# Kernel optimization log

Hardware: AMD Instinct MI355X
Metric: run time of the kernel (lower is better)

Reference implementation:

```python
import jax, jax.numpy as jnp
import numpy as np

B, T, N, F = 32, 256, 68, 64
NUM_LAYERS = 3
EPS = 1e-5


def _build_adjacency(n):
    a = np.zeros((n, n), dtype=np.float32)
    i = np.arange(n)
    a[i[1:], i[1:] - 1] = 1.0
    a[i[:-1], i[:-1] + 1] = 1.0
    return jnp.asarray(a)


def setup_inputs() -> dict:
    key = jax.random.key(0)
    ks = jax.random.split(key, 10)
    x = jax.random.normal(ks[0], (B, T, N, 2), dtype=jnp.float32)
    adj = _build_adjacency(N)  # (N, N) tridiagonal buffer (not trainable)
    W_enc = jax.random.normal(ks[1], (2, F), dtype=jnp.float32) * 0.5
    b_enc = jax.random.normal(ks[2], (F,), dtype=jnp.float32) * 0.05
    W_gnn = jax.random.normal(ks[3], (NUM_LAYERS, F, F), dtype=jnp.float32) * (1.0 / np.sqrt(F))
    b_gnn = jax.random.normal(ks[4], (NUM_LAYERS, F), dtype=jnp.float32) * 0.05
    gamma = jnp.ones((NUM_LAYERS, F), dtype=jnp.float32)
    beta = jnp.zeros((NUM_LAYERS, F), dtype=jnp.float32)
    W1 = jax.random.normal(ks[5], (F, 32), dtype=jnp.float32) * (1.0 / np.sqrt(F))
    b1 = jax.random.normal(ks[6], (32,), dtype=jnp.float32) * 0.05
    W2 = jax.random.normal(ks[7], (32, 1), dtype=jnp.float32) * (1.0 / np.sqrt(32))
    b2 = jax.random.normal(ks[8], (1,), dtype=jnp.float32) * 0.05
    return {"landmarks_sequence": x, "adj": adj, "W_enc": W_enc, "b_enc": b_enc,
            "W_gnn": W_gnn, "b_gnn": b_gnn, "gamma": gamma, "beta": beta,
            "W1": W1, "b1": b1, "W2": W2, "b2": b2}


def _layernorm(z, g, b):
    mu = jnp.mean(z, axis=-1, keepdims=True)
    var = jnp.mean(jnp.square(z - mu), axis=-1, keepdims=True)
    return (z - mu) * jax.lax.rsqrt(var + EPS) * g + b


def reference(landmarks_sequence, adj, W_enc, b_enc, W_gnn, b_gnn, gamma, beta, W1, b1, W2, b2):
    # Vectorize the torch per-timestep Python loop: all T timesteps at once.
    # node encoder: (B,T,N,2) -> (B,T,N,F)
    h = landmarks_sequence @ W_enc + b_enc
    for l in range(NUM_LAYERS):
        # neighbor aggregation via tridiagonal adjacency (same math as dense NxN matmul)
        agg = jnp.einsum('nm,btmf->btnf', adj, h)
        z = jax.nn.relu(agg @ W_gnn[l] + b_gnn[l])
        h = _layernorm(z, gamma[l], beta[l]) + h  # residual
    pooled = jnp.mean(h, axis=2)                  # AdaptiveAvgPool1d(1) over nodes -> (B,T,F)
    logits = jax.nn.relu(pooled @ W1 + b1) @ W2 + b2  # (B,T,1)
    return jnp.mean(logits, axis=1).squeeze(-1)       # mean over T, squeeze -> (B,)
```

## Files before the change

### kernel.cpp

```cpp
#include <hip/hip_runtime.h>

#define B_SZ 32
#define T_SZ 256
#define N_NODES 68
#define NLAYERS 3
#define EPS 1e-5f

#define HP 72
#define HROWS 70
#define NS 4

typedef _Float16 f16x8 __attribute__((ext_vector_type(8)));
typedef _Float16 f16x4 __attribute__((ext_vector_type(4)));
typedef _Float16 f16x2 __attribute__((ext_vector_type(2)));
typedef __fp16   fp16v2 __attribute__((ext_vector_type(2)));
typedef float    f32x4 __attribute__((ext_vector_type(4)));
typedef int      v2i   __attribute__((ext_vector_type(2)));

__device__ __forceinline__ float red16(float x) {
#if __has_builtin(__builtin_amdgcn_permlane16_swap)
    v2i r = __builtin_amdgcn_permlane16_swap(__float_as_int(x), __float_as_int(x),
                                             false, false);
    return __int_as_float(r[0]) + __int_as_float(r[1]);
#else
    return x + __shfl_xor(x, 16);
#endif
}
__device__ __forceinline__ float red32(float x) {
#if __has_builtin(__builtin_amdgcn_permlane32_swap)
    v2i r = __builtin_amdgcn_permlane32_swap(__float_as_int(x), __float_as_int(x),
                                             false, false);
    return __int_as_float(r[0]) + __int_as_float(r[1]);
#else
    return x + __shfl_xor(x, 32);
#endif
}

__device__ __forceinline__ f16x2 pack2(float a, float b) {
    fp16v2 p = __builtin_amdgcn_cvt_pkrtz(a, b);
    return __builtin_bit_cast(f16x2, p);
}
__device__ __forceinline__ f16x4 pack4(float a, float b, float c, float d) {
    f16x2 lo = pack2(a, b);
    f16x2 hi = pack2(c, d);
    f16x4 o;
    o[0] = lo[0]; o[1] = lo[1]; o[2] = hi[0]; o[3] = hi[1];
    return o;
}

__global__ void prep_k(const float* __restrict__ W, const float* __restrict__ W1,
                       const float* __restrict__ gamma, const float* __restrict__ beta,
                       _Float16* __restrict__ Wt, float* __restrict__ W1t,
                       _Float16* __restrict__ gb16, float* __restrict__ out) {
    int idx = blockIdx.x * 256 + threadIdx.x;
    if (idx < 12288) {
        int l = idx >> 12, r = idx & 4095;
        int m = r >> 6, k = r & 63;
        Wt[(l << 12) + (m << 6) + k] = (_Float16)W[(l << 12) + (k << 6) + m];
    } else if (idx < 14336) {
        int r = idx - 12288;
        int j = r >> 6, f = r & 63;
        W1t[r] = W1[f * 32 + j];
    } else if (idx < 14720) {
        int r = idx - 14336;
        gb16[r] = (_Float16)(r < 192 ? gamma[r] : beta[r - 192]);
    } else if (idx < 14752) {
        out[idx - 14720] = 0.f;
    }
}

__global__ __launch_bounds__(64, 1)
void gnn_wave(const float* __restrict__ x,
              const float* __restrict__ W_enc, const float* __restrict__ b_enc,
              const _Float16* __restrict__ Wt, const float* __restrict__ b_gnn,
              const _Float16* __restrict__ gb16,
              const float* __restrict__ W1t, const float* __restrict__ b1,
              const float* __restrict__ W2, const float* __restrict__ b2,
              float* __restrict__ out)
{
    __shared__ _Float16 hsh[NS][HROWS * HP];

    const int lane = threadIdx.x;
    const int l15  = lane & 15;
    const int quad = lane >> 4;

    const int g0 = blockIdx.x * NS;
    _Float16* hS[NS];
    const float* xpS[NS];
    #pragma unroll
    for (int s = 0; s < NS; ++s) {
        hS[s]  = hsh[s];
        xpS[s] = x + (size_t)(g0 + s) * (N_NODES * 2);
    }

    if (lane < 36) {
        #pragma unroll
        for (int s = 0; s < NS; ++s) {
            ((unsigned*)hS[s])[lane] = 0u;
            ((unsigned*)(hS[s] + 69 * HP))[lane] = 0u;
        }
    }

    {
        const f32x4 we0 = ((const f32x4*)W_enc)[l15];
        const f32x4 we1 = ((const f32x4*)(W_enc + 64))[l15];
        const f32x4 be  = ((const f32x4*)b_enc)[l15];
        #pragma unroll
        for (int i = 0; i < 17; ++i) {
            int n = i * 4 + quad;
            #pragma unroll
            for (int s = 0; s < NS; ++s) {
                float2 xv = *(const float2*)&xpS[s][n * 2];
                f32x4 hv = xv.x * we0 + xv.y * we1 + be;
                *(f16x4*)&hS[s][(n + 1) * HP + l15 * 4] =
                    pack4(hv[0], hv[1], hv[2], hv[3]);
            }
        }
    }

    #pragma unroll 1
    for (int l = 0; l < NLAYERS; ++l) {
        const _Float16* WtL = Wt + (l << 12);

        __builtin_amdgcn_sched_barrier(0);

        f16x8 a0[4], a1[4];
        f32x4 bgv[4];
        f16x4 gmv[4], bbv[4];
        #pragma unroll
        for (int k = 0; k < 4; ++k) {
            a0[k]  = *(const f16x8*)&WtL[(k * 16 + l15) * 64 + quad * 8];
            a1[k]  = *(const f16x8*)&WtL[(k * 16 + l15) * 64 + 32 + quad * 8];
            bgv[k] = *(const f32x4*)&b_gnn[l * 64 + k * 16 + quad * 4];
            gmv[k] = *(const f16x4*)&gb16[l * 64 + k * 16 + quad * 4];
            bbv[k] = *(const f16x4*)&gb16[192 + l * 64 + k * 16 + quad * 4];
        }

        f16x8 cA0[NS], cA1[NS], nA0[NS], nA1[NS];
        #pragma unroll
        for (int s = 0; s < NS; ++s) {
            const _Float16* q = hS[s] + l15 * HP + quad * 8;
            cA0[s] = *(const f16x8*)q; cA1[s] = *(const f16x8*)(q + 32);
        }

        #pragma unroll
        for (int t = 0; t < 5; ++t) {
            const int n  = t * 16 + l15;
            const int nc = (t == 4) ? (n > 67 ? 67 : n) : n;
            const int rc = nc + 1;

            f16x8 C0[NS], C1[NS];
            f16x4 hv[NS][4];
            #pragma unroll
            for (int s = 0; s < NS; ++s) {
                const _Float16* p = hS[s] + nc * HP + quad * 8;
                C0[s] = *(const f16x8*)(p + 2 * HP);
                C1[s] = *(const f16x8*)(p + 2 * HP + 32);
                #pragma unroll
                for (int k = 0; k < 4; ++k)
                    hv[s][k] = *(const f16x4*)&hS[s][rc * HP + k * 16 + quad * 4];
            }
            if (t < 4) {
                int nn  = (t + 1) * 16 + l15;
                int nnc = (t == 3) ? (nn > 67 ? 67 : nn) : nn;
                #pragma unroll
                for (int s = 0; s < NS; ++s) {
                    const _Float16* q = hS[s] + nnc * HP + quad * 8;
                    nA0[s] = *(const f16x8*)q; nA1[s] = *(const f16x8*)(q + 32);
                }
            }

            f32x4 acc[NS][4];
            #pragma unroll
            for (int s = 0; s < NS; ++s) {
                f16x8 b0 = cA0[s] + C0[s];
                f16x8 b1 = cA1[s] + C1[s];
                #pragma unroll
                for (int k = 0; k < 4; ++k) {
                    f32x4 z = bgv[k];
                    z = __builtin_amdgcn_mfma_f32_16x16x32_f16(a0[k], b0, z, 0, 0, 0);
                    z = __builtin_amdgcn_mfma_f32_16x16x32_f16(a1[k], b1, z, 0, 0, 0);
                    acc[s][k] = z;
                }
            }

            float S[NS], Q[NS], mu[NS], rs[NS], m2[NS];
            #pragma unroll
            for (int s = 0; s < NS; ++s) { S[s] = 0.f; Q[s] = 0.f; }
            #pragma unroll
            for (int s = 0; s < NS; ++s) {
                #pragma unroll
                for (int k = 0; k < 4; ++k) {
                    f32x4 z = acc[s][k];
                    #pragma unroll
                    for (int i = 0; i < 4; ++i) {
                        float v = fmaxf(z[i], 0.f);
                        z[i] = v; S[s] += v; Q[s] = fmaf(v, v, Q[s]);
                    }
                    acc[s][k] = z;
                }
            }
            #pragma unroll
            for (int s = 0; s < NS; ++s) { S[s] = red16(S[s]); Q[s] = red16(Q[s]); }
            #pragma unroll
            for (int s = 0; s < NS; ++s) { S[s] = red32(S[s]); Q[s] = red32(Q[s]); }
            #pragma unroll
            for (int s = 0; s < NS; ++s) {
                mu[s] = S[s] * (1.f / 64.f);
                rs[s] = rsqrtf(fmaf(-mu[s], mu[s], Q[s] * (1.f / 64.f)) + EPS);
                m2[s] = -mu[s] * rs[s];
            }

            __builtin_amdgcn_sched_barrier(0x47F);

            if (t < 4 || l15 < 4) {
                #pragma unroll
                for (int s = 0; s < NS; ++s) {
                    #pragma unroll
                    for (int k = 0; k < 4; ++k) {
                        f16x4 th = pack4(fmaf(acc[s][k][0], rs[s], m2[s]),
                                         fmaf(acc[s][k][1], rs[s], m2[s]),
                                         fmaf(acc[s][k][2], rs[s], m2[s]),
                                         fmaf(acc[s][k][3], rs[s], m2[s]));
                        f16x4 r = th * gmv[k] + bbv[k] + hv[s][k];
                        *(f16x4*)&hS[s][rc * HP + k * 16 + quad * 4] = r;
                    }
                }
            }

            #pragma unroll
            for (int s = 0; s < NS; ++s) { cA0[s] = nA0[s]; cA1[s] = nA1[s]; }
        }
    }

    __builtin_amdgcn_sched_barrier(0);

    f32x4 ps[NS];
    #pragma unroll
    for (int s = 0; s < NS; ++s) {
        f32x4 pp0 = {0.f,0.f,0.f,0.f}, pp1 = {0.f,0.f,0.f,0.f};
        f32x4 pp2 = {0.f,0.f,0.f,0.f}, pp3 = {0.f,0.f,0.f,0.f};
        #pragma unroll
        for (int i = 0; i < 17; ++i) {
            f16x4 v = *(const f16x4*)&hS[s][(i * 4 + quad + 1) * HP + l15 * 4];
            f32x4 a = {(float)v[0], (float)v[1], (float)v[2], (float)v[3]};
            if ((i & 3) == 0) pp0 += a;
            else if ((i & 3) == 1) pp1 += a;
            else if ((i & 3) == 2) pp2 += a;
            else pp3 += a;
        }
        ps[s] = (pp0 + pp1) + (pp2 + pp3);
    }
    #pragma unroll
    for (int s = 0; s < NS; ++s)
        #pragma unroll
        for (int i = 0; i < 4; ++i)
            ps[s][i] = red32(red16(ps[s][i])) * (1.f / (float)N_NODES);

    __builtin_amdgcn_sched_barrier(0x47F);
    if (quad == 0) {
        #pragma unroll
        for (int s = 0; s < NS; ++s)
            *(f32x4*)&((float*)hS[s])[l15 * 4] = ps[s];
    }
    __builtin_amdgcn_sched_barrier(0x47F);

    {
        const int j = lane & 31, hf = lane >> 5;
        const float b1j = hf ? 0.f : b1[j];
        float a[NS];
        #pragma unroll
        for (int s = 0; s < NS; ++s) a[s] = b1j;
        const float* wrow = W1t + j * 64 + hf * 32;
        #pragma unroll
        for (int k = 0; k < 8; ++k) {
            f32x4 pw = *(const f32x4*)&wrow[k * 4];
            #pragma unroll
            for (int s = 0; s < NS; ++s) {
                f32x4 pv = *(const f32x4*)&((float*)hS[s])[hf * 32 + k * 4];
                a[s] = fmaf(pv[0], pw[0], a[s]); a[s] = fmaf(pv[1], pw[1], a[s]);
                a[s] = fmaf(pv[2], pw[2], a[s]); a[s] = fmaf(pv[3], pw[3], a[s]);
            }
        }
        const float w2j = W2[j];
        float v = 0.f;
        #pragma unroll
        for (int s = 0; s < NS; ++s)
            v += fmaxf(red32(a[s]), 0.f) * w2j;
        v += __shfl_xor(v, 16);
        v += __shfl_xor(v, 8);
        v += __shfl_xor(v, 4);
        v += __shfl_xor(v, 2);
        v += __shfl_xor(v, 1);
        if (lane == 0)
            atomicAdd(out + (g0 >> 8), (v + (float)NS * b2[0]) * (1.f / (float)T_SZ));
    }
}

extern "C" void kernel_launch(void* const* d_in, const int* in_sizes, int n_in,
                              void* d_out, int out_size, void* d_ws, size_t ws_size,
                              hipStream_t stream) {
    const float* x     = (const float*)d_in[0];
    const float* W_enc = (const float*)d_in[2];
    const float* b_enc = (const float*)d_in[3];
    const float* W_gnn = (const float*)d_in[4];
    const float* b_gnn = (const float*)d_in[5];
    const float* gamma = (const float*)d_in[6];
    const float* beta  = (const float*)d_in[7];
    const float* W1    = (const float*)d_in[8];
    const float* b1    = (const float*)d_in[9];
    const float* W2    = (const float*)d_in[10];
    const float* b2    = (const float*)d_in[11];
    float* out = (float*)d_out;

    _Float16* Wt   = (_Float16*)d_ws;
    float*    W1t  = (float*)((char*)d_ws + (1 << 15));
    _Float16* gb16 = (_Float16*)((char*)d_ws + 49152);

    prep_k<<<58, 256, 0, stream>>>(W_gnn, W1, gamma, beta, Wt, W1t, gb16, out);

    const int n_graphs = B_SZ * T_SZ;
    gnn_wave<<<n_graphs / NS, 64, 0, stream>>>(x, W_enc, b_enc, Wt, b_gnn,
                                               gb16, W1t, b1, W2, b2, out);
}
```

Before: 152.7 us.

## Permute weight output rows for contiguous f16x8 LDS access and pack f32x2 LayerNorm math

Permutes the output-feature order of the transposed GNN weights so each lane's four MFMA accumulator tiles map to 16 contiguous features. This lets the residual h reads, gamma/beta loads and LayerNorm writes use two 128-bit LDS accesses instead of four 64-bit ones. The ReLU/sum/sumsq and normalize FMAs are rewritten as packed f32x2 vector ops, and rsqrtf is replaced with the raw v_rsq_f32 instruction. The cost is a more intricate index mapping that must stay consistent between prep and the main kernel, plus slightly lower rsqrt accuracy.

```diff
diff --git a/kernel.cpp b/kernel.cpp
--- a/kernel.cpp
+++ b/kernel.cpp
@@ -15,6 +15,7 @@
 typedef _Float16 f16x2 __attribute__((ext_vector_type(2)));
 typedef __fp16   fp16v2 __attribute__((ext_vector_type(2)));
 typedef float    f32x4 __attribute__((ext_vector_type(4)));
+typedef float    f32x2 __attribute__((ext_vector_type(2)));
 typedef int      v2i   __attribute__((ext_vector_type(2)));
 
 __device__ __forceinline__ float red16(float x) {
@@ -36,6 +37,12 @@
 #endif
 }
 
+__device__ __forceinline__ float fast_rsqrt(float v) {
+    float r;
+    asm("v_rsq_f32 %0, %1" : "=v"(r) : "v"(v));
+    return r;
+}
+
 __device__ __forceinline__ f16x2 pack2(float a, float b) {
     fp16v2 p = __builtin_amdgcn_cvt_pkrtz(a, b);
     return __builtin_bit_cast(f16x2, p);
@@ -46,6 +53,16 @@
     f16x4 o;
     o[0] = lo[0]; o[1] = lo[1]; o[2] = hi[0]; o[3] = hi[1];
     return o;
+}
+__device__ __forceinline__ f16x8 cat8(f16x4 a, f16x4 b) {
+    return __builtin_shufflevector(a, b, 0, 1, 2, 3, 4, 5, 6, 7);
+}
+__device__ __forceinline__ f32x2 vmax0(f32x2 p) {
+#if __has_builtin(__builtin_elementwise_max)
+    return __builtin_elementwise_max(p, (f32x2){0.f, 0.f});
+#else
+    f32x2 r; r[0] = fmaxf(p[0], 0.f); r[1] = fmaxf(p[1], 0.f); return r;
+#endif
 }
 
 __global__ void prep_k(const float* __restrict__ W, const float* __restrict__ W1,
@@ -56,7 +73,8 @@
     if (idx < 12288) {
         int l = idx >> 12, r = idx & 4095;
         int m = r >> 6, k = r & 63;
-        Wt[(l << 12) + (m << 6) + k] = (_Float16)W[(l << 12) + (k << 6) + m];
+        int fm = ((m >> 2) & 3) * 16 + (m >> 4) * 4 + (m & 3);
+        Wt[(l << 12) + (m << 6) + k] = (_Float16)W[(l << 12) + (k << 6) + fm];
     } else if (idx < 14336) {
         int r = idx - 12288;
         int j = r >> 6, f = r & 63;
@@ -126,15 +144,16 @@
 
         f16x8 a0[4], a1[4];
         f32x4 bgv[4];
-        f16x4 gmv[4], bbv[4];
         #pragma unroll
         for (int k = 0; k < 4; ++k) {
             a0[k]  = *(const f16x8*)&WtL[(k * 16 + l15) * 64 + quad * 8];
             a1[k]  = *(const f16x8*)&WtL[(k * 16 + l15) * 64 + 32 + quad * 8];
-            bgv[k] = *(const f32x4*)&b_gnn[l * 64 + k * 16 + quad * 4];
-            gmv[k] = *(const f16x4*)&gb16[l * 64 + k * 16 + quad * 4];
-            bbv[k] = *(const f16x4*)&gb16[192 + l * 64 + k * 16 + quad * 4];
-        }
+            bgv[k] = *(const f32x4*)&b_gnn[l * 64 + quad * 16 + k * 4];
+        }
+        const f16x8 gmA = *(const f16x8*)&gb16[l * 64 + quad * 16];
+        const f16x8 gmB = *(const f16x8*)&gb16[l * 64 + quad * 16 + 8];
+        const f16x8 bbA = *(const f16x8*)&gb16[192 + l * 64 + quad * 16];
+        const f16x8 bbB = *(const f16x8*)&gb16[192 + l * 64 + quad * 16 + 8];
 
         f16x8 cA0[NS], cA1[NS], nA0[NS], nA1[NS];
         #pragma unroll
@@ -149,16 +168,14 @@
             const int nc = (t == 4) ? (n > 67 ? 67 : n) : n;
             const int rc = nc + 1;
 
-            f16x8 C0[NS], C1[NS];
-            f16x4 hv[NS][4];
+            f16x8 C0[NS], C1[NS], hvA[NS], hvB[NS];
             #pragma unroll
             for (int s = 0; s < NS; ++s) {
                 const _Float16* p = hS[s] + nc * HP + quad * 8;
                 C0[s] = *(const f16x8*)(p + 2 * HP);
                 C1[s] = *(const f16x8*)(p + 2 * HP + 32);
-                #pragma unroll
-                for (int k = 0; k < 4; ++k)
-                    hv[s][k] = *(const f16x4*)&hS[s][rc * HP + k * 16 + quad * 4];
+                hvA[s] = *(const f16x8*)&hS[s][rc * HP + quad * 16];
+                hvB[s] = *(const f16x8*)&hS[s][rc * HP + quad * 16 + 8];
             }
             if (t < 4) {
                 int nn  = (t + 1) * 16 + l15;
@@ -184,30 +201,26 @@
                 }
             }
 
-            float S[NS], Q[NS], mu[NS], rs[NS], m2[NS];
-            #pragma unroll
-            for (int s = 0; s < NS; ++s) { S[s] = 0.f; Q[s] = 0.f; }
-            #pragma unroll
-            for (int s = 0; s < NS; ++s) {
+            float mu[NS], rs[NS], m2[NS];
+            #pragma unroll
+            for (int s = 0; s < NS; ++s) {
+                f32x2 S2 = {0.f, 0.f}, Q2 = {0.f, 0.f};
                 #pragma unroll
                 for (int k = 0; k < 4; ++k) {
                     f32x4 z = acc[s][k];
-                    #pragma unroll
-                    for (int i = 0; i < 4; ++i) {
-                        float v = fmaxf(z[i], 0.f);
-                        z[i] = v; S[s] += v; Q[s] = fmaf(v, v, Q[s]);
-                    }
-                    acc[s][k] = z;
+                    f32x2 p0 = vmax0((f32x2){z[0], z[1]});
+                    f32x2 p1 = vmax0((f32x2){z[2], z[3]});
+                    S2 += p0; S2 += p1;
+                    Q2 = p0 * p0 + Q2;
+                    Q2 = p1 * p1 + Q2;
+                    acc[s][k] = __builtin_shufflevector(p0, p1, 0, 1, 2, 3);
                 }
-            }
-            #pragma unroll
-            for (int s = 0; s < NS; ++s) { S[s] = red16(S[s]); Q[s] = red16(Q[s]); }
-            #pragma unroll
-            for (int s = 0; s < NS; ++s) { S[s] = red32(S[s]); Q[s] = red32(Q[s]); }
-            #pragma unroll
-            for (int s = 0; s < NS; ++s) {
-                mu[s] = S[s] * (1.f / 64.f);
-                rs[s] = rsqrtf(fmaf(-mu[s], mu[s], Q[s] * (1.f / 64.f)) + EPS);
+                float S = S2[0] + S2[1];
+                float Q = Q2[0] + Q2[1];
+                S = red16(S); Q = red16(Q);
+                S = red32(S); Q = red32(Q);
+                mu[s] = S * (1.f / 64.f);
+                rs[s] = fast_rsqrt(fmaf(-mu[s], mu[s], Q * (1.f / 64.f)) + EPS);
                 m2[s] = -mu[s] * rs[s];
             }
 
@@ -216,15 +229,18 @@
             if (t < 4 || l15 < 4) {
                 #pragma unroll
                 for (int s = 0; s < NS; ++s) {
+                    f32x2 rs2 = {rs[s], rs[s]}, m22 = {m2[s], m2[s]};
+                    f16x4 th[4];
                     #pragma unroll
                     for (int k = 0; k < 4; ++k) {
-                        f16x4 th = pack4(fmaf(acc[s][k][0], rs[s], m2[s]),
-                                         fmaf(acc[s][k][1], rs[s], m2[s]),
-                                         fmaf(acc[s][k][2], rs[s], m2[s]),
-                                         fmaf(acc[s][k][3], rs[s], m2[s]));
-                        f16x4 r = th * gmv[k] + bbv[k] + hv[s][k];
-                        *(f16x4*)&hS[s][rc * HP + k * 16 + quad * 4] = r;
+                        f32x2 u0 = (f32x2){acc[s][k][0], acc[s][k][1]} * rs2 + m22;
+                        f32x2 u1 = (f32x2){acc[s][k][2], acc[s][k][3]} * rs2 + m22;
+                        th[k] = pack4(u0[0], u0[1], u1[0], u1[1]);
                     }
+                    f16x8 rA = cat8(th[0], th[1]) * gmA + bbA + hvA[s];
+                    f16x8 rB = cat8(th[2], th[3]) * gmB + bbB + hvB[s];
+                    *(f16x8*)&hS[s][rc * HP + quad * 16]     = rA;
+                    *(f16x8*)&hS[s][rc * HP + quad * 16 + 8] = rB;
                 }
             }
 
```

Measured after the change: 145.3 us, median of 2. -4.9%, faster.
